# Performance work log

Hardware: AMD Instinct MI355X
Metric: run time of the kernel (lower is better)

The kernel has to match this reference:

```python
import jax, jax.numpy as jnp
import numpy as np

K = 3  # neighbors for knn_interpolate


def _knn_interpolate(x, pos, pos_skip, B, k):
    """PyG knn_interpolate with equal-sized batches.
    x: [N_coarse, C], pos: [N_coarse, 3], pos_skip: [N_fine, 3].
    """
    C = x.shape[1]
    xb = x.reshape(B, -1, C)          # [B, nc, C]
    pb = pos.reshape(B, -1, 3)        # [B, nc, 3]
    qb = pos_skip.reshape(B, -1, 3)   # [B, nf, 3]

    def per_cloud(xf, pf, qf):
        # squared distances [nf, nc]
        d2 = jnp.sum((qf[:, None, :] - pf[None, :, :]) ** 2, axis=-1)
        neg_d2k, idx = jax.lax.top_k(-d2, k)          # k smallest distances
        d2k = -neg_d2k                                # [nf, k]
        w = 1.0 / jnp.clip(d2k, 1e-16)                # inverse-distance weights
        w = jax.lax.stop_gradient(w)                  # PyG computes weights under no_grad
        feats = xf[idx]                               # [nf, k, C] gather
        return jnp.sum(w[..., None] * feats, axis=1) / jnp.sum(w, axis=1, keepdims=True)

    y = jax.vmap(per_cloud)(xb, pb, qb)               # [B, nf, C]
    return y.reshape(-1, C)


def setup_inputs() -> dict:
    key = jax.random.key(0)
    ks = jax.random.split(key, 8)
    B, n_coarse, n_fine = 16, 1024, 4096
    C_in, C_skip, C_mid, C_out = 256, 128, 256, 256
    x = jax.random.normal(ks[0], (B * n_coarse, C_in), jnp.float32)
    pos = jax.random.uniform(ks[1], (B * n_coarse, 3), jnp.float32)
    x_skip = jax.random.normal(ks[2], (B * n_fine, C_skip), jnp.float32)
    pos_skip = jax.random.uniform(ks[3], (B * n_fine, 3), jnp.float32)
    batch = jnp.repeat(jnp.arange(B, dtype=jnp.int64), n_coarse)
    batch_skip = jnp.repeat(jnp.arange(B, dtype=jnp.int64), n_fine)
    seed_idx = jnp.arange(B * n_coarse, dtype=jnp.int64)
    seed_idx_skip = jnp.arange(B * n_fine, dtype=jnp.int64)
    W1 = jax.random.normal(ks[4], (C_in + C_skip, C_mid), jnp.float32) * 0.05
    b1 = jnp.zeros((C_mid,), jnp.float32)
    W2 = jax.random.normal(ks[5], (C_mid, C_out), jnp.float32) * 0.05
    b2 = jnp.zeros((C_out,), jnp.float32)
    return {"x": x, "pos": pos, "batch": batch, "seed_idx": seed_idx,
            "x_skip": x_skip, "pos_skip": pos_skip, "batch_skip": batch_skip,
            "seed_idx_skip": seed_idx_skip, "W1": W1, "b1": b1, "W2": W2, "b2": b2}


def reference(x, pos, batch, seed_idx, x_skip, pos_skip, batch_skip, seed_idx_skip,
              W1, b1, W2, b2):
    B = int(batch[-1]) + 1  # equal-sized contiguous clouds
    y = _knn_interpolate(x, pos, pos_skip, B, K)      # [N_fine, C_in]
    h = jnp.concatenate([y, x_skip], axis=1)          # [N_fine, C_in+C_skip]
    h = jax.nn.relu(h @ W1 + b1)                      # MLP layer 1
    out = jax.nn.relu(h @ W2 + b2)                    # MLP layer 2
    return (out, pos_skip, batch_skip)
```

## Files before the change

### kernel.cpp

```cpp
#include <hip/hip_runtime.h>
#include <hip/hip_bf16.h>

#define NB    16
#define NC    1024
#define NF    4096
#define NFINE (NB*NF)
#define CIN   256
#define CSKIP 128
#define KH    (CIN+CSKIP)
#define CMID  256
#define COUT  256

typedef __attribute__((ext_vector_type(8))) short short8;
typedef __attribute__((ext_vector_type(4))) float f32x4;
typedef __attribute__((ext_vector_type(4))) unsigned int u32x4;

__global__ __launch_bounds__(256)
void bin_kernel(const float* __restrict__ pos,
                float* __restrict__ gp,
                int* __restrict__ gcs)
{
    __shared__ int cnt[512];
    __shared__ float lx[NC], ly[NC], lz[NC];
    __shared__ short lcell[NC];
    const int b = blockIdx.x, t = threadIdx.x;
    for (int i = t; i < 512; i += 256) cnt[i] = 0;
    __syncthreads();
    const float* pc = pos + (size_t)b*NC*3;
    #pragma unroll
    for (int u = 0; u < 4; ++u) {
        int i = t + u*256;
        float x = pc[3*i+0], y = pc[3*i+1], z = pc[3*i+2];
        int cx = min(7, (int)(x*8.0f));
        int cy = min(7, (int)(y*8.0f));
        int cz = min(7, (int)(z*8.0f));
        int c = (cz*8 + cy)*8 + cx;
        lx[i] = x; ly[i] = y; lz[i] = z; lcell[i] = (short)c;
        atomicAdd(&cnt[c], 1);
    }
    __syncthreads();
    if (t < 64) {
        int v[8]; int s = 0;
        #pragma unroll
        for (int u = 0; u < 8; ++u) { v[u] = cnt[t*8+u]; s += v[u]; }
        int pfx = s;
        #pragma unroll
        for (int m = 1; m < 64; m <<= 1) {
            int o = __shfl_up(pfx, m);
            if (t >= m) pfx += o;
        }
        pfx -= s;
        #pragma unroll
        for (int u = 0; u < 8; ++u) {
            gcs[b*513 + t*8+u] = pfx;
            cnt[t*8+u] = pfx;
            pfx += v[u];
        }
        if (t == 63) gcs[b*513 + 512] = NC;
    }
    __syncthreads();
    #pragma unroll
    for (int u = 0; u < 4; ++u) {
        int i = t + u*256;
        int c = lcell[i];
        int dst = atomicAdd(&cnt[c], 1);
        f32x4 v; v[0] = lx[i]; v[1] = ly[i]; v[2] = lz[i]; v[3] = __int_as_float(i);
        *(f32x4*)&gp[(size_t)(b*NC + dst)*4] = v;
    }
}

#define KQPB 32

#define INS(d, j) do {                                        \
    bool c2 = (d) < dB, c1 = (d) < dA, c0 = (d) < d0;         \
    dB = c1 ? dA : (c2 ? (d) : dB);                           \
    iB = c1 ? iA : (c2 ? (j) : iB);                           \
    dA = c0 ? d0 : (c1 ? (d) : dA);                           \
    iA = c0 ? i0 : (c1 ? (j) : iA);                           \
    d0 = c0 ? (d) : d0;                                       \
    i0 = c0 ? (j) : i0;                                       \
} while (0)

#define SCAN(JS, JE) for (int j = (JS) + g; j < (JE); j += 8) {        \
    const f32x4 p = *(const f32x4*)&pp[j][0];                          \
    float fx = qx - p[0], fy = qy - p[1], fz = qz - p[2];              \
    float dd = fx*fx + fy*fy + fz*fz;                                  \
    INS(dd, j);                                                        \
}

#define MERGE8() do {                                                          \
    _Pragma("unroll")                                                          \
    for (int mm = 1; mm < 8; mm <<= 1) {                                       \
        float e0 = __shfl_xor(d0, mm), e1 = __shfl_xor(dA, mm), e2 = __shfl_xor(dB, mm); \
        int   f0 = __shfl_xor(i0, mm), f1 = __shfl_xor(iA, mm), f2 = __shfl_xor(iB, mm); \
        INS(e0, f0); INS(e1, f1); INS(e2, f2);                                 \
    }                                                                          \
} while (0)

__global__ __launch_bounds__(256)
void knn_grid_kernel(const float* __restrict__ pos_skip,
                     const float* __restrict__ gp,
                     const int* __restrict__ gcs,
                     int* __restrict__ widx, float* __restrict__ wval)
{
    __shared__ __align__(16) float pp[NC][4];
    __shared__ unsigned short cs[513];
    const int bpc = NF/KQPB;
    const int b  = blockIdx.x / bpc;
    const int qb = blockIdx.x % bpc;
    const int t  = threadIdx.x;
    for (int i = t; i < NC; i += 256)
        *(f32x4*)&pp[i][0] = *(const f32x4*)&gp[(size_t)(b*NC + i)*4];
    for (int i = t; i < 513; i += 256) cs[i] = (unsigned short)gcs[b*513 + i];
    __syncthreads();

    const int g  = t & 7;
    const int ql = t >> 3;
    const int q  = b*NF + qb*KQPB + ql;
    const float qx = pos_skip[(size_t)q*3+0];
    const float qy = pos_skip[(size_t)q*3+1];
    const float qz = pos_skip[(size_t)q*3+2];
    const int cx = min(7, (int)(qx*8.0f));
    const int cy = min(7, (int)(qy*8.0f));
    const int cz = min(7, (int)(qz*8.0f));

    float d0 = 3.0e38f, dA = 3.0e38f, dB = 3.0e38f;
    int   i0 = 0,       iA = 0,       iB = 0;

    const int xlo = max(cx-1,0), xhi = min(cx+1,7);
    const int ylo = max(cy-1,0), yhi = min(cy+1,7);
    const int zlo = max(cz-1,0), zhi = min(cz+1,7);
    #pragma unroll
    for (int r = 0; r < 9; ++r) {
        const int z = cz - 1 + r/3;
        const int y = cy - 1 + r%3;
        const bool ok = ((unsigned)z < 8u) & ((unsigned)y < 8u);
        const int rb = (z*8 + y)*8;
        int js = 0, je = 0;
        if (ok) { js = cs[rb + xlo]; je = cs[rb + xhi + 1]; }
        SCAN(js, je);
    }
    MERGE8();

    float m1 = 3.0e38f;
    if (xlo > 0) m1 = fminf(m1, qx - xlo*0.125f);
    if (xhi < 7) m1 = fminf(m1, (xhi+1)*0.125f - qx);
    if (ylo > 0) m1 = fminf(m1, qy - ylo*0.125f);
    if (yhi < 7) m1 = fminf(m1, (yhi+1)*0.125f - qy);
    if (zlo > 0) m1 = fminf(m1, qz - zlo*0.125f);
    if (zhi < 7) m1 = fminf(m1, (zhi+1)*0.125f - qz);

    if (dB > m1*m1) {
        const float s0 = d0, s1 = dA, s2 = dB;
        const int   t0 = i0, t1 = iA, t2 = iB;
        d0 = dA = dB = 3.0e38f; i0 = iA = iB = 0;

        const int xlo2 = max(cx-2,0), xhi2 = min(cx+2,7);
        const int ylo2 = max(cy-2,0), yhi2 = min(cy+2,7);
        const int zlo2 = max(cz-2,0), zhi2 = min(cz+2,7);
        for (int z = zlo2; z <= zhi2; ++z)
        for (int y = ylo2; y <= yhi2; ++y) {
            const int rb = (z*8 + y)*8;
            const bool inner_zy = (z >= zlo && z <= zhi && y >= ylo && y <= yhi);
            int jsA, jeA, jsB, jeB;
            if (inner_zy) {
                jsA = cs[rb + xlo2]; jeA = cs[rb + xlo];
                jsB = cs[rb + xhi + 1]; jeB = cs[rb + xhi2 + 1];
            } else {
                jsA = cs[rb + xlo2]; jeA = cs[rb + xhi2 + 1];
                jsB = 0; jeB = 0;
            }
            SCAN(jsA, jeA);
            SCAN(jsB, jeB);
        }
        MERGE8();
        INS(s0, t0); INS(s1, t1); INS(s2, t2);

        float m2 = 3.0e38f;
        if (xlo2 > 0) m2 = fminf(m2, qx - xlo2*0.125f);
        if (xhi2 < 7) m2 = fminf(m2, (xhi2+1)*0.125f - qx);
        if (ylo2 > 0) m2 = fminf(m2, qy - ylo2*0.125f);
        if (yhi2 < 7) m2 = fminf(m2, (yhi2+1)*0.125f - qy);
        if (zlo2 > 0) m2 = fminf(m2, qz - zlo2*0.125f);
        if (zhi2 < 7) m2 = fminf(m2, (zhi2+1)*0.125f - qz);
        if (dB > m2*m2) {
            const float u0 = d0, u1 = dA, u2 = dB;
            const int   v0 = i0, v1 = iA, v2 = iB;
            d0 = dA = dB = 3.0e38f; i0 = iA = iB = 0;
            for (int j = g; j < NC; j += 8) {
                const f32x4 p = *(const f32x4*)&pp[j][0];
                int pcx = min(7, (int)(p[0]*8.0f));
                int pcy = min(7, (int)(p[1]*8.0f));
                int pcz = min(7, (int)(p[2]*8.0f));
                if (pcx >= xlo2 && pcx <= xhi2 && pcy >= ylo2 && pcy <= yhi2 &&
                    pcz >= zlo2 && pcz <= zhi2) continue;
                float fx = qx - p[0], fy = qy - p[1], fz = qz - p[2];
                float dd = fx*fx + fy*fy + fz*fz;
                INS(dd, j);
            }
            MERGE8();
            INS(u0, v0); INS(u1, v1); INS(u2, v2);
        }
    }

    if (g == 0) {
        const int o0 = __float_as_int(pp[i0][3]);
        const int o1 = __float_as_int(pp[iA][3]);
        const int o2 = __float_as_int(pp[iB][3]);
        float w0 = 1.0f / fmaxf(d0, 1e-16f);
        float w1 = 1.0f / fmaxf(dA, 1e-16f);
        float w2 = 1.0f / fmaxf(dB, 1e-16f);
        float inv = 1.0f / (w0 + w1 + w2);
        widx[q*3+0] = b*NC + o0;  wval[q*3+0] = w0*inv;
        widx[q*3+1] = b*NC + o1;  wval[q*3+1] = w1*inv;
        widx[q*3+2] = b*NC + o2;  wval[q*3+2] = w2*inv;
    }
}

__global__ __launch_bounds__(256)
void prep_weights(const float* __restrict__ W1, const float* __restrict__ W2,
                  __hip_bfloat16* __restrict__ W1t, __hip_bfloat16* __restrict__ W2t)
{
    int e = blockIdx.x*256 + threadIdx.x;
    if (e < CMID*KH) {
        int n = e / KH, k = e % KH;
        W1t[e] = __float2bfloat16(W1[(size_t)k*CMID + n]);
    }
    int e2 = e - CMID*KH;
    if (e2 >= 0 && e2 < COUT*CMID) {
        int n = e2 / CMID, k = e2 % CMID;
        W2t[e2] = __float2bfloat16(W2[(size_t)k*COUT + n]);
    }
}

__global__ __launch_bounds__(512, 4)
void mlp_fused(const float* __restrict__ x,
               const float* __restrict__ x_skip,
               const int* __restrict__ widx,
               const float* __restrict__ wval,
               const __hip_bfloat16* __restrict__ W1t,
               const float* __restrict__ b1,
               const __hip_bfloat16* __restrict__ W2t,
               const float* __restrict__ b2,
               float* __restrict__ out)
{
    __shared__ __align__(16) short As[64][64];
    __shared__ __align__(16) short Bs[256][64];
    __shared__ __align__(16) short Hs[64][256];
    const int nwg = gridDim.x;
    const int tile = (blockIdx.x & 7)*(nwg >> 3) + (blockIdx.x >> 3);
    const int m0 = tile * 64;

    const int t = threadIdx.x;
    const int wave = t >> 6, lane = t & 63;
    const int wm = wave >> 2, wn = wave & 3;
    const int rl = lane & 15, kq = lane >> 4;
    const short* B1r = (const short*)W1t;
    const short* B2r = (const short*)W2t;

    const int ar = t >> 3;
    const int ac = t & 7;

    const int gr = m0 + ar;
    const int j0 = widx[gr*3+0], j1 = widx[gr*3+1], j2 = widx[gr*3+2];
    const float w0 = wval[gr*3+0], w1 = wval[gr*3+1], w2 = wval[gr*3+2];

    f32x4 rA[6];
    u32x4 rB[4];

    #define LOADB(BP, KT, K0) do {                                             \
        _Pragma("unroll")                                                      \
        for (int i = 0; i < 4; ++i) {                                          \
            const int ch = t + i*512;                                          \
            const int rr = ch >> 3, cc = ch & 7;                               \
            rB[i] = *(const u32x4*)&(BP)[(size_t)rr*(KT) + (K0) + cc*8];       \
        }                                                                      \
    } while (0)

    #define LOADA1(K0) do {                                                   \
        if ((K0) < CIN) {                                                      \
            const int k = (K0) + ac*8;                                         \
            const float* p0 = &x[(size_t)j0*CIN + k];                          \
            const float* p1 = &x[(size_t)j1*CIN + k];                          \
            const float* p2 = &x[(size_t)j2*CIN + k];                          \
            rA[0] = *(const f32x4*)p0; rA[1] = *(const f32x4*)(p0+4);          \
            rA[2] = *(const f32x4*)p1; rA[3] = *(const f32x4*)(p1+4);          \
            rA[4] = *(const f32x4*)p2; rA[5] = *(const f32x4*)(p2+4);          \
        } else {                                                               \
            const int k = (K0) + ac*8 - CIN;                                   \
            const float* sp = &x_skip[(size_t)gr*CSKIP + k];                   \
            rA[0] = *(const f32x4*)sp; rA[1] = *(const f32x4*)(sp+4);          \
        }                                                                      \
    } while (0)

    f32x4 acc[2][4] = {};

    LOADA1(0); LOADB(B1r, KH, 0);

    #pragma unroll
    for (int s = 0; s < 6; ++s) {
        const int k0 = s * 64;
        __syncthreads();
        {
            short8 sv;
            if (k0 < CIN) {
                #pragma unroll
                for (int u = 0; u < 2; ++u) {
                    f32x4 a = rA[u], bq = rA[2+u], c = rA[4+u];
                    #pragma unroll
                    for (int e = 0; e < 4; ++e) {
                        float v = w0*a[e] + w1*bq[e] + w2*c[e];
                        __hip_bfloat16 bb = __float2bfloat16(v);
                        ((short*)&sv)[u*4+e] = *(short*)&bb;
                    }
                }
            } else {
                #pragma unroll
                for (int u = 0; u < 2; ++u) {
                    f32x4 a = rA[u];
                    #pragma unroll
                    for (int e = 0; e < 4; ++e) {
                        __hip_bfloat16 bb = __float2bfloat16(a[e]);
                        ((short*)&sv)[u*4+e] = *(short*)&bb;
                    }
                }
            }
            *(short8*)&As[ar][(ac ^ (ar&7))*8] = sv;
        }
        #pragma unroll
        for (int i = 0; i < 4; ++i) {
            const int ch = t + i*512;
            const int rr = ch >> 3, cc = ch & 7;
            *(u32x4*)&Bs[rr][(cc ^ (rr&7))*8] = rB[i];
        }
        __syncthreads();
        if (s < 5) { LOADA1(k0 + 64); LOADB(B1r, KH, k0 + 64); }
        else       { LOADB(B2r, CMID, 0); }
        #pragma unroll
        for (int kh = 0; kh < 2; ++kh) {
            const int kc = kh*4 + kq;
            short8 af[2], bf[4];
            #pragma unroll
            for (int mf = 0; mf < 2; ++mf)
                af[mf] = *(const short8*)&As[wm*32 + mf*16 + rl][(kc ^ (rl&7))*8];
            #pragma unroll
            for (int nf = 0; nf < 4; ++nf)
                bf[nf] = *(const short8*)&Bs[wn*64 + nf*16 + rl][(kc ^ (rl&7))*8];
            #pragma unroll
            for (int mf = 0; mf < 2; ++mf)
            #pragma unroll
            for (int nf = 0; nf < 4; ++nf)
                acc[mf][nf] = __builtin_amdgcn_mfma_f32_16x16x32_bf16(af[mf], bf[nf], acc[mf][nf], 0,0,0);
        }
    }

    #pragma unroll
    for (int mf = 0; mf < 2; ++mf)
    #pragma unroll
    for (int nf = 0; nf < 4; ++nf) {
        const int col = wn*64 + nf*16 + rl;
        const float bv = b1[col];
        #pragma unroll
        for (int i = 0; i < 4; ++i) {
            const int row = wm*32 + mf*16 + kq*4 + i;
            float v = fmaxf(acc[mf][nf][i] + bv, 0.0f);
            __hip_bfloat16 bb = __float2bfloat16(v);
            Hs[row][((col >> 3) ^ (row & 7))*8 + (col & 7)] = *(short*)&bb;
        }
    }
    __syncthreads();

    f32x4 acc2[2][4] = {};
    #pragma unroll
    for (int s = 0; s < 4; ++s) {
        if (s > 0) __syncthreads();
        #pragma unroll
        for (int i = 0; i < 4; ++i) {
            const int ch = t + i*512;
            const int rr = ch >> 3, cc = ch & 7;
            *(u32x4*)&Bs[rr][(cc ^ (rr&7))*8] = rB[i];
        }
        __syncthreads();
        if (s < 3) LOADB(B2r, CMID, (s+1)*64);
        #pragma unroll
        for (int kh = 0; kh < 2; ++kh) {
            const int kcl = kh*4 + kq;
            const int kca = s*8 + kcl;
            short8 af[2], bf[4];
            #pragma unroll
            for (int mf = 0; mf < 2; ++mf)
                af[mf] = *(const short8*)&Hs[wm*32 + mf*16 + rl][(kca ^ (rl&7))*8];
            #pragma unroll
            for (int nf = 0; nf < 4; ++nf)
                bf[nf] = *(const short8*)&Bs[wn*64 + nf*16 + rl][(kcl ^ (rl&7))*8];
            #pragma unroll
            for (int mf = 0; mf < 2; ++mf)
            #pragma unroll
            for (int nf = 0; nf < 4; ++nf)
                acc2[mf][nf] = __builtin_amdgcn_mfma_f32_16x16x32_bf16(af[mf], bf[nf], acc2[mf][nf], 0,0,0);
        }
    }
    #undef LOADA1
    #undef LOADB

    #pragma unroll
    for (int mf = 0; mf < 2; ++mf)
    #pragma unroll
    for (int nf = 0; nf < 4; ++nf) {
        const int col = wn*64 + nf*16 + rl;
        const float bv = b2[col];
        #pragma unroll
        for (int i = 0; i < 4; ++i) {
            const int row = m0 + wm*32 + mf*16 + kq*4 + i;
            out[(size_t)row*COUT + col] = fmaxf(acc2[mf][nf][i] + bv, 0.0f);
        }
    }
}

__global__ __launch_bounds__(256)
void tail_kernel(const float* __restrict__ pos_skip, float* __restrict__ out)
{
    int e = blockIdx.x*256 + threadIdx.x;
    if (e < NFINE*3) out[(size_t)NFINE*COUT + e] = pos_skip[e];
    if (e < NFINE)   out[(size_t)NFINE*COUT + (size_t)NFINE*3 + e] = (float)(e / NF);
}

extern "C" void kernel_launch(void* const* d_in, const int* in_sizes, int n_in,
                              void* d_out, int out_size, void* d_ws, size_t ws_size,
                              hipStream_t stream) {
    const float* x        = (const float*)d_in[0];
    const float* pos      = (const float*)d_in[1];
    const float* x_skip   = (const float*)d_in[4];
    const float* pos_skip = (const float*)d_in[5];
    const float* W1       = (const float*)d_in[8];
    const float* b1       = (const float*)d_in[9];
    const float* W2       = (const float*)d_in[10];
    const float* b2       = (const float*)d_in[11];
    float* out = (float*)d_out;
    char* ws = (char*)d_ws;

    int*            widx = (int*)  (ws + 0);
    float*          wval = (float*)(ws + 786432);
    __hip_bfloat16* W1t  = (__hip_bfloat16*)(ws + 1572864);
    __hip_bfloat16* W2t  = (__hip_bfloat16*)(ws + 1769472);
    float*          gp   = (float*)(ws + 1900544);
    int*            gcs  = (int*)  (ws + 2162688);

    hipLaunchKernelGGL(bin_kernel, dim3(NB), dim3(256), 0, stream,
                       pos, gp, gcs);
    hipLaunchKernelGGL(knn_grid_kernel, dim3(NB*(NF/KQPB)), dim3(256), 0, stream,
                       pos_skip, gp, gcs, widx, wval);
    hipLaunchKernelGGL(prep_weights, dim3((CMID*KH + COUT*CMID + 255)/256), dim3(256), 0, stream,
                       W1, W2, W1t, W2t);
    hipLaunchKernelGGL(mlp_fused, dim3(NFINE/64), dim3(512), 0, stream,
                       x, x_skip, widx, wval, W1t, b1, W2t, b2, out);
    hipLaunchKernelGGL(tail_kernel, dim3((NFINE*3 + 255)/256), dim3(256), 0, stream,
                       pos_skip, out);
}
```

Baseline: 76.58 us.

## Double-buffer register prefetch in fused MLP and enlarge KNN query blocks

The fused MLP kernel now keeps two register sets for A and B tiles, prefetching two k-steps ahead instead of one, so global gather latency is hidden across more MFMA work. The launch-bounds occupancy hint drops from 4 to 2 blocks to make room for the extra registers. Separately, the KNN kernel handles 64 queries per 512-thread block instead of 32 per 256, halving the number of blocks that each reload the cloud's points into shared memory. The cost is lower MLP occupancy and fewer, larger KNN blocks.

```diff
diff --git a/kernel.cpp b/kernel.cpp
--- a/kernel.cpp
+++ b/kernel.cpp
@@ -69,7 +69,7 @@
     }
 }
 
-#define KQPB 32
+#define KQPB 64
 
 #define INS(d, j) do {                                        \
     bool c2 = (d) < dB, c1 = (d) < dA, c0 = (d) < d0;         \
@@ -97,7 +97,7 @@
     }                                                                          \
 } while (0)
 
-__global__ __launch_bounds__(256)
+__global__ __launch_bounds__(512)
 void knn_grid_kernel(const float* __restrict__ pos_skip,
                      const float* __restrict__ gp,
                      const int* __restrict__ gcs,
@@ -109,9 +109,9 @@
     const int b  = blockIdx.x / bpc;
     const int qb = blockIdx.x % bpc;
     const int t  = threadIdx.x;
-    for (int i = t; i < NC; i += 256)
+    for (int i = t; i < NC; i += 512)
         *(f32x4*)&pp[i][0] = *(const f32x4*)&gp[(size_t)(b*NC + i)*4];
-    for (int i = t; i < 513; i += 256) cs[i] = (unsigned short)gcs[b*513 + i];
+    for (int i = t; i < 513; i += 512) cs[i] = (unsigned short)gcs[b*513 + i];
     __syncthreads();
 
     const int g  = t & 7;
@@ -233,7 +233,7 @@
     }
 }
 
-__global__ __launch_bounds__(512, 4)
+__global__ __launch_bounds__(512, 2)
 void mlp_fused(const float* __restrict__ x,
                const float* __restrict__ x_skip,
                const int* __restrict__ widx,
@@ -265,94 +265,109 @@
     const int j0 = widx[gr*3+0], j1 = widx[gr*3+1], j2 = widx[gr*3+2];
     const float w0 = wval[gr*3+0], w1 = wval[gr*3+1], w2 = wval[gr*3+2];
 
-    f32x4 rA[6];
-    u32x4 rB[4];
-
-    #define LOADB(BP, KT, K0) do {                                             \
+    f32x4 rA0[6], rA1[6];
+    u32x4 rB0[4], rB1[4];
+
+    #define LOADB(RB, BP, KT, K0) do {                                         \
         _Pragma("unroll")                                                      \
         for (int i = 0; i < 4; ++i) {                                          \
             const int ch = t + i*512;                                          \
             const int rr = ch >> 3, cc = ch & 7;                               \
-            rB[i] = *(const u32x4*)&(BP)[(size_t)rr*(KT) + (K0) + cc*8];       \
-        }                                                                      \
-    } while (0)
-
-    #define LOADA1(K0) do {                                                   \
+            RB[i] = *(const u32x4*)&(BP)[(size_t)rr*(KT) + (K0) + cc*8];       \
+        }                                                                      \
+    } while (0)
+
+    #define LOADA1(RA, K0) do {                                               \
         if ((K0) < CIN) {                                                      \
             const int k = (K0) + ac*8;                                         \
             const float* p0 = &x[(size_t)j0*CIN + k];                          \
             const float* p1 = &x[(size_t)j1*CIN + k];                          \
             const float* p2 = &x[(size_t)j2*CIN + k];                          \
-            rA[0] = *(const f32x4*)p0; rA[1] = *(const f32x4*)(p0+4);          \
-            rA[2] = *(const f32x4*)p1; rA[3] = *(const f32x4*)(p1+4);          \
-            rA[4] = *(const f32x4*)p2; rA[5] = *(const f32x4*)(p2+4);          \
+            RA[0] = *(const f32x4*)p0; RA[1] = *(const f32x4*)(p0+4);          \
+            RA[2] = *(const f32x4*)p1; RA[3] = *(const f32x4*)(p1+4);          \
+            RA[4] = *(const f32x4*)p2; RA[5] = *(const f32x4*)(p2+4);          \
         } else {                                                               \
             const int k = (K0) + ac*8 - CIN;                                   \
             const float* sp = &x_skip[(size_t)gr*CSKIP + k];                   \
-            rA[0] = *(const f32x4*)sp; rA[1] = *(const f32x4*)(sp+4);          \
+            RA[0] = *(const f32x4*)sp; RA[1] = *(const f32x4*)(sp+4);          \
+        }                                                                      \
+    } while (0)
+
+    #define STAGE_A(RA, K0) do {                                               \
+        short8 sv;                                                             \
+        if ((K0) < CIN) {                                                      \
+            _Pragma("unroll")                                                  \
+            for (int u = 0; u < 2; ++u) {                                      \
+                f32x4 a = RA[u], bq = RA[2+u], c = RA[4+u];                    \
+                _Pragma("unroll")                                              \
+                for (int e = 0; e < 4; ++e) {                                  \
+                    float v = w0*a[e] + w1*bq[e] + w2*c[e];                    \
+                    __hip_bfloat16 bb = __float2bfloat16(v);                   \
+                    ((short*)&sv)[u*4+e] = *(short*)&bb;                       \
+                }                                                              \
+            }                                                                  \
+        } else {                                                               \
+            _Pragma("unroll")                                                  \
+            for (int u = 0; u < 2; ++u) {                                      \
+                f32x4 a = RA[u];                                               \
+                _Pragma("unroll")                                              \
+                for (int e = 0; e < 4; ++e) {                                  \
+                    __hip_bfloat16 bb = __float2bfloat16(a[e]);                \
+                    ((short*)&sv)[u*4+e] = *(short*)&bb;                       \
+                }                                                              \
+            }                                                                  \
+        }                                                                      \
+        *(short8*)&As[ar][(ac ^ (ar&7))*8] = sv;                               \
+    } while (0)
+
+    #define STAGE_B(RB) do {                                                   \
+        _Pragma("unroll")                                                      \
+        for (int i = 0; i < 4; ++i) {                                          \
+            const int ch = t + i*512;                                          \
+            const int rr = ch >> 3, cc = ch & 7;                               \
+            *(u32x4*)&Bs[rr][(cc ^ (rr&7))*8] = RB[i];                         \
         }                                                                      \
     } while (0)
 
     f32x4 acc[2][4] = {};
 
-    LOADA1(0); LOADB(B1r, KH, 0);
-
-    #pragma unroll
-    for (int s = 0; s < 6; ++s) {
-        const int k0 = s * 64;
-        __syncthreads();
-        {
-            short8 sv;
-            if (k0 < CIN) {
-                #pragma unroll
-                for (int u = 0; u < 2; ++u) {
-                    f32x4 a = rA[u], bq = rA[2+u], c = rA[4+u];
-                    #pragma unroll
-                    for (int e = 0; e < 4; ++e) {
-                        float v = w0*a[e] + w1*bq[e] + w2*c[e];
-                        __hip_bfloat16 bb = __float2bfloat16(v);
-                        ((short*)&sv)[u*4+e] = *(short*)&bb;
-                    }
-                }
-            } else {
-                #pragma unroll
-                for (int u = 0; u < 2; ++u) {
-                    f32x4 a = rA[u];
-                    #pragma unroll
-                    for (int e = 0; e < 4; ++e) {
-                        __hip_bfloat16 bb = __float2bfloat16(a[e]);
-                        ((short*)&sv)[u*4+e] = *(short*)&bb;
-                    }
-                }
-            }
-            *(short8*)&As[ar][(ac ^ (ar&7))*8] = sv;
-        }
-        #pragma unroll
-        for (int i = 0; i < 4; ++i) {
-            const int ch = t + i*512;
-            const int rr = ch >> 3, cc = ch & 7;
-            *(u32x4*)&Bs[rr][(cc ^ (rr&7))*8] = rB[i];
-        }
-        __syncthreads();
-        if (s < 5) { LOADA1(k0 + 64); LOADB(B1r, KH, k0 + 64); }
-        else       { LOADB(B2r, CMID, 0); }
-        #pragma unroll
-        for (int kh = 0; kh < 2; ++kh) {
-            const int kc = kh*4 + kq;
-            short8 af[2], bf[4];
-            #pragma unroll
-            for (int mf = 0; mf < 2; ++mf)
-                af[mf] = *(const short8*)&As[wm*32 + mf*16 + rl][(kc ^ (rl&7))*8];
-            #pragma unroll
-            for (int nf = 0; nf < 4; ++nf)
-                bf[nf] = *(const short8*)&Bs[wn*64 + nf*16 + rl][(kc ^ (rl&7))*8];
-            #pragma unroll
-            for (int mf = 0; mf < 2; ++mf)
-            #pragma unroll
-            for (int nf = 0; nf < 4; ++nf)
-                acc[mf][nf] = __builtin_amdgcn_mfma_f32_16x16x32_bf16(af[mf], bf[nf], acc[mf][nf], 0,0,0);
-        }
-    }
+    #define MFMA1() do {                                                       \
+        _Pragma("unroll")                                                      \
+        for (int kh = 0; kh < 2; ++kh) {                                       \
+            const int kc = kh*4 + kq;                                          \
+            short8 af[2], bf[4];                                               \
+            _Pragma("unroll")                                                  \
+            for (int mf = 0; mf < 2; ++mf)                                     \
+                af[mf] = *(const short8*)&As[wm*32 + mf*16 + rl][(kc ^ (rl&7))*8]; \
+            _Pragma("unroll")                                                  \
+            for (int nf = 0; nf < 4; ++nf)                                     \
+                bf[nf] = *(const short8*)&Bs[wn*64 + nf*16 + rl][(kc ^ (rl&7))*8]; \
+            _Pragma("unroll")                                                  \
+            for (int mf = 0; mf < 2; ++mf)                                     \
+            _Pragma("unroll")                                                  \
+            for (int nf = 0; nf < 4; ++nf)                                     \
+                acc[mf][nf] = __builtin_amdgcn_mfma_f32_16x16x32_bf16(af[mf], bf[nf], acc[mf][nf], 0,0,0); \
+        }                                                                      \
+    } while (0)
+
+    LOADA1(rA0, 0);   LOADB(rB0, B1r, KH, 0);
+    LOADA1(rA1, 64);  LOADB(rB1, B1r, KH, 64);
+
+    #define PHASE1_STEP(S, RA, RB, LOADNEXT) do {                              \
+        __syncthreads();                                                       \
+        STAGE_A(RA, (S)*64);                                                   \
+        STAGE_B(RB);                                                           \
+        __syncthreads();                                                       \
+        LOADNEXT                                                               \
+        MFMA1();                                                               \
+    } while (0)
+
+    PHASE1_STEP(0, rA0, rB0, { LOADA1(rA0, 128); LOADB(rB0, B1r, KH, 128); });
+    PHASE1_STEP(1, rA1, rB1, { LOADA1(rA1, 192); LOADB(rB1, B1r, KH, 192); });
+    PHASE1_STEP(2, rA0, rB0, { LOADA1(rA0, 256); LOADB(rB0, B1r, KH, 256); });
+    PHASE1_STEP(3, rA1, rB1, { LOADA1(rA1, 320); LOADB(rB1, B1r, KH, 320); });
+    PHASE1_STEP(4, rA0, rB0, { LOADB(rB0, B2r, CMID, 0);   });
+    PHASE1_STEP(5, rA1, rB1, { LOADB(rB1, B2r, CMID, 64);  });
 
     #pragma unroll
     for (int mf = 0; mf < 2; ++mf)
@@ -371,37 +386,39 @@
     __syncthreads();
 
     f32x4 acc2[2][4] = {};
-    #pragma unroll
-    for (int s = 0; s < 4; ++s) {
-        if (s > 0) __syncthreads();
-        #pragma unroll
-        for (int i = 0; i < 4; ++i) {
-            const int ch = t + i*512;
-            const int rr = ch >> 3, cc = ch & 7;
-            *(u32x4*)&Bs[rr][(cc ^ (rr&7))*8] = rB[i];
-        }
-        __syncthreads();
-        if (s < 3) LOADB(B2r, CMID, (s+1)*64);
-        #pragma unroll
-        for (int kh = 0; kh < 2; ++kh) {
-            const int kcl = kh*4 + kq;
-            const int kca = s*8 + kcl;
-            short8 af[2], bf[4];
-            #pragma unroll
-            for (int mf = 0; mf < 2; ++mf)
-                af[mf] = *(const short8*)&Hs[wm*32 + mf*16 + rl][(kca ^ (rl&7))*8];
-            #pragma unroll
-            for (int nf = 0; nf < 4; ++nf)
-                bf[nf] = *(const short8*)&Bs[wn*64 + nf*16 + rl][(kcl ^ (rl&7))*8];
-            #pragma unroll
-            for (int mf = 0; mf < 2; ++mf)
-            #pragma unroll
-            for (int nf = 0; nf < 4; ++nf)
-                acc2[mf][nf] = __builtin_amdgcn_mfma_f32_16x16x32_bf16(af[mf], bf[nf], acc2[mf][nf], 0,0,0);
-        }
-    }
-    #undef LOADA1
-    #undef LOADB
+
+    #define MFMA2(S2) do {                                                     \
+        _Pragma("unroll")                                                      \
+        for (int kh = 0; kh < 2; ++kh) {                                       \
+            const int kcl = kh*4 + kq;                                         \
+            const int kca = (S2)*8 + kcl;                                      \
+            short8 af[2], bf[4];                                               \
+            _Pragma("unroll")                                                  \
+            for (int mf = 0; mf < 2; ++mf)                                     \
+                af[mf] = *(const short8*)&Hs[wm*32 + mf*16 + rl][(kca ^ (rl&7))*8]; \
+            _Pragma("unroll")                                                  \
+            for (int nf = 0; nf < 4; ++nf)                                     \
+                bf[nf] = *(const short8*)&Bs[wn*64 + nf*16 + rl][(kcl ^ (rl&7))*8]; \
+            _Pragma("unroll")                                                  \
+            for (int mf = 0; mf < 2; ++mf)                                     \
+            _Pragma("unroll")                                                  \
+            for (int nf = 0; nf < 4; ++nf)                                     \
+                acc2[mf][nf] = __builtin_amdgcn_mfma_f32_16x16x32_bf16(af[mf], bf[nf], acc2[mf][nf], 0,0,0); \
+        }                                                                      \
+    } while (0)
+
+    #define PHASE2_STEP(S2, RB, LOADNEXT, FIRSTBAR) do {                       \
+        FIRSTBAR                                                               \
+        STAGE_B(RB);                                                           \
+        __syncthreads();                                                       \
+        LOADNEXT                                                               \
+        MFMA2(S2);                                                             \
+    } while (0)
+
+    PHASE2_STEP(0, rB0, { LOADB(rB0, B2r, CMID, 128); }, );
+    PHASE2_STEP(1, rB1, { LOADB(rB1, B2r, CMID, 192); }, __syncthreads(););
+    PHASE2_STEP(2, rB0, { }, __syncthreads(););
+    PHASE2_STEP(3, rB1, { }, __syncthreads(););
 
     #pragma unroll
     for (int mf = 0; mf < 2; ++mf)
@@ -415,6 +432,14 @@
             out[(size_t)row*COUT + col] = fmaxf(acc2[mf][nf][i] + bv, 0.0f);
         }
     }
+    #undef LOADB
+    #undef LOADA1
+    #undef STAGE_A
+    #undef STAGE_B
+    #undef MFMA1
+    #undef MFMA2
+    #undef PHASE1_STEP
+    #undef PHASE2_STEP
 }
 
 __global__ __launch_bounds__(256)
@@ -448,7 +473,7 @@
 
     hipLaunchKernelGGL(bin_kernel, dim3(NB), dim3(256), 0, stream,
                        pos, gp, gcs);
-    hipLaunchKernelGGL(knn_grid_kernel, dim3(NB*(NF/KQPB)), dim3(256), 0, stream,
+    hipLaunchKernelGGL(knn_grid_kernel, dim3(NB*(NF/KQPB)), dim3(512), 0, stream,
                        pos_skip, gp, gcs, widx, wval);
     hipLaunchKernelGGL(prep_weights, dim3((CMID*KH + COUT*CMID + 255)/256), dim3(256), 0, stream,
                        W1, W2, W1t, W2t);
```

Result: slower. 83.50 us (+9.0%).

## Split fused MLP into two GEMM kernels and front-load gathered A tile

Applied to the files above, without the earlier changes.

Unfuses the MLP kernel into gemm1, which gathers and interpolates the full 64x384 A tile into shared memory up front and writes bf16 h1 to workspace, and gemm2, which uses 128-row tiles over h1. The KNN kernel now handles 64 queries per 512-thread block. The intent is to overlap the gather latency better, raise MFMA tile efficiency in the second GEMM and cut barrier and register pressure. The cost is an extra global round trip for h1 (32 MB of bf16 traffic) plus one more kernel launch.

```diff
diff --git a/kernel.cpp b/kernel.cpp
--- a/kernel.cpp
+++ b/kernel.cpp
@@ -69,7 +69,7 @@
     }
 }
 
-#define KQPB 32
+#define KQPB 64
 
 #define INS(d, j) do {                                        \
     bool c2 = (d) < dB, c1 = (d) < dA, c0 = (d) < d0;         \
@@ -97,7 +97,7 @@
     }                                                                          \
 } while (0)
 
-__global__ __launch_bounds__(256)
+__global__ __launch_bounds__(512)
 void knn_grid_kernel(const float* __restrict__ pos_skip,
                      const float* __restrict__ gp,
                      const int* __restrict__ gcs,
@@ -109,9 +109,9 @@
     const int b  = blockIdx.x / bpc;
     const int qb = blockIdx.x % bpc;
     const int t  = threadIdx.x;
-    for (int i = t; i < NC; i += 256)
+    for (int i = t; i < NC; i += 512)
         *(f32x4*)&pp[i][0] = *(const f32x4*)&gp[(size_t)(b*NC + i)*4];
-    for (int i = t; i < 513; i += 256) cs[i] = (unsigned short)gcs[b*513 + i];
+    for (int i = t; i < 513; i += 512) cs[i] = (unsigned short)gcs[b*513 + i];
     __syncthreads();
 
     const int g  = t & 7;
@@ -233,20 +233,17 @@
     }
 }
 
-__global__ __launch_bounds__(512, 4)
-void mlp_fused(const float* __restrict__ x,
-               const float* __restrict__ x_skip,
-               const int* __restrict__ widx,
-               const float* __restrict__ wval,
-               const __hip_bfloat16* __restrict__ W1t,
-               const float* __restrict__ b1,
-               const __hip_bfloat16* __restrict__ W2t,
-               const float* __restrict__ b2,
-               float* __restrict__ out)
+__global__ __launch_bounds__(512, 2)
+void gemm1_kernel(const float* __restrict__ x,
+                  const float* __restrict__ x_skip,
+                  const int* __restrict__ widx,
+                  const float* __restrict__ wval,
+                  const __hip_bfloat16* __restrict__ W1t,
+                  const float* __restrict__ b1,
+                  __hip_bfloat16* __restrict__ h1)
 {
-    __shared__ __align__(16) short As[64][64];
+    __shared__ __align__(16) short Af[64][KH];
     __shared__ __align__(16) short Bs[256][64];
-    __shared__ __align__(16) short Hs[64][256];
     const int nwg = gridDim.x;
     const int tile = (blockIdx.x & 7)*(nwg >> 3) + (blockIdx.x >> 3);
     const int m0 = tile * 64;
@@ -256,77 +253,182 @@
     const int wm = wave >> 2, wn = wave & 3;
     const int rl = lane & 15, kq = lane >> 4;
     const short* B1r = (const short*)W1t;
-    const short* B2r = (const short*)W2t;
 
     const int ar = t >> 3;
     const int ac = t & 7;
+    const int sw = ac ^ (ar & 7);
 
     const int gr = m0 + ar;
     const int j0 = widx[gr*3+0], j1 = widx[gr*3+1], j2 = widx[gr*3+2];
     const float w0 = wval[gr*3+0], w1 = wval[gr*3+1], w2 = wval[gr*3+2];
 
-    f32x4 rA[6];
+    f32x4 pa[6], pb[6];
+
+    #define LOADC(P, C) do {                                                   \
+        if ((C) < 4) {                                                         \
+            const int k = ((C)*8 + ac)*8;                                      \
+            const float* p0 = &x[(size_t)j0*CIN + k];                          \
+            const float* p1 = &x[(size_t)j1*CIN + k];                          \
+            const float* p2 = &x[(size_t)j2*CIN + k];                          \
+            P[0] = *(const f32x4*)p0; P[1] = *(const f32x4*)(p0+4);            \
+            P[2] = *(const f32x4*)p1; P[3] = *(const f32x4*)(p1+4);            \
+            P[4] = *(const f32x4*)p2; P[5] = *(const f32x4*)(p2+4);            \
+        } else {                                                               \
+            const int k = ((C)*8 + ac)*8 - CIN;                                \
+            const float* sp = &x_skip[(size_t)gr*CSKIP + k];                   \
+            P[0] = *(const f32x4*)sp; P[1] = *(const f32x4*)(sp+4);            \
+        }                                                                      \
+    } while (0)
+
+    #define STOREC(P, C) do {                                                  \
+        short8 sv;                                                             \
+        if ((C) < 4) {                                                         \
+            _Pragma("unroll")                                                  \
+            for (int u = 0; u < 2; ++u) {                                      \
+                f32x4 a = P[u], bq = P[2+u], c_ = P[4+u];                      \
+                _Pragma("unroll")                                              \
+                for (int e = 0; e < 4; ++e) {                                  \
+                    float v = w0*a[e] + w1*bq[e] + w2*c_[e];                   \
+                    __hip_bfloat16 bb = __float2bfloat16(v);                   \
+                    ((short*)&sv)[u*4+e] = *(short*)&bb;                       \
+                }                                                              \
+            }                                                                  \
+        } else {                                                               \
+            _Pragma("unroll")                                                  \
+            for (int u = 0; u < 2; ++u) {                                      \
+                f32x4 a = P[u];                                                \
+                _Pragma("unroll")                                              \
+                for (int e = 0; e < 4; ++e) {                                  \
+                    __hip_bfloat16 bb = __float2bfloat16(a[e]);                \
+                    ((short*)&sv)[u*4+e] = *(short*)&bb;                       \
+                }                                                              \
+            }                                                                  \
+        }                                                                      \
+        *(short8*)&Af[ar][((C)*8 + sw)*8] = sv;                                \
+    } while (0)
+
     u32x4 rB[4];
-
-    #define LOADB(BP, KT, K0) do {                                             \
+    #define LOADB(K0) do {                                                     \
         _Pragma("unroll")                                                      \
         for (int i = 0; i < 4; ++i) {                                          \
             const int ch = t + i*512;                                          \
             const int rr = ch >> 3, cc = ch & 7;                               \
-            rB[i] = *(const u32x4*)&(BP)[(size_t)rr*(KT) + (K0) + cc*8];       \
+            rB[i] = *(const u32x4*)&B1r[(size_t)rr*KH + (K0) + cc*8];          \
         }                                                                      \
     } while (0)
 
-    #define LOADA1(K0) do {                                                   \
-        if ((K0) < CIN) {                                                      \
-            const int k = (K0) + ac*8;                                         \
-            const float* p0 = &x[(size_t)j0*CIN + k];                          \
-            const float* p1 = &x[(size_t)j1*CIN + k];                          \
-            const float* p2 = &x[(size_t)j2*CIN + k];                          \
-            rA[0] = *(const f32x4*)p0; rA[1] = *(const f32x4*)(p0+4);          \
-            rA[2] = *(const f32x4*)p1; rA[3] = *(const f32x4*)(p1+4);          \
-            rA[4] = *(const f32x4*)p2; rA[5] = *(const f32x4*)(p2+4);          \
-        } else {                                                               \
-            const int k = (K0) + ac*8 - CIN;                                   \
-            const float* sp = &x_skip[(size_t)gr*CSKIP + k];                   \
-            rA[0] = *(const f32x4*)sp; rA[1] = *(const f32x4*)(sp+4);          \
+    #define STAGE_B() do {                                                     \
+        _Pragma("unroll")                                                      \
+        for (int i = 0; i < 4; ++i) {                                          \
+            const int ch = t + i*512;                                          \
+            const int rr = ch >> 3, cc = ch & 7;                               \
+            *(u32x4*)&Bs[rr][(cc ^ (rr&7))*8] = rB[i];                         \
         }                                                                      \
     } while (0)
 
+    LOADC(pa, 0); LOADC(pb, 1);
+    STOREC(pa, 0); LOADC(pa, 2);
+    STOREC(pb, 1); LOADC(pb, 3);
+    STOREC(pa, 2); LOADC(pa, 4);
+    STOREC(pb, 3); LOADC(pb, 5);
+    STOREC(pa, 4);
+    STOREC(pb, 5);
+    LOADB(0);
+
     f32x4 acc[2][4] = {};
 
-    LOADA1(0); LOADB(B1r, KH, 0);
-
     #pragma unroll
     for (int s = 0; s < 6; ++s) {
-        const int k0 = s * 64;
         __syncthreads();
-        {
-            short8 sv;
-            if (k0 < CIN) {
-                #pragma unroll
-                for (int u = 0; u < 2; ++u) {
-                    f32x4 a = rA[u], bq = rA[2+u], c = rA[4+u];
-                    #pragma unroll
-                    for (int e = 0; e < 4; ++e) {
-                        float v = w0*a[e] + w1*bq[e] + w2*c[e];
-                        __hip_bfloat16 bb = __float2bfloat16(v);
-                        ((short*)&sv)[u*4+e] = *(short*)&bb;
-                    }
-                }
-            } else {
-                #pragma unroll
-                for (int u = 0; u < 2; ++u) {
-                    f32x4 a = rA[u];
-                    #pragma unroll
-                    for (int e = 0; e < 4; ++e) {
-                        __hip_bfloat16 bb = __float2bfloat16(a[e]);
-                        ((short*)&sv)[u*4+e] = *(short*)&bb;
-                    }
-                }
-            }
-            *(short8*)&As[ar][(ac ^ (ar&7))*8] = sv;
-        }
+        STAGE_B();
+        __syncthreads();
+        if (s < 5) LOADB((s+1)*64);
+        #pragma unroll
+        for (int kh = 0; kh < 2; ++kh) {
+            const int w_ = kh*4 + kq;
+            short8 af[2], bf[4];
+            #pragma unroll
+            for (int mf = 0; mf < 2; ++mf)
+                af[mf] = *(const short8*)&Af[wm*32 + mf*16 + rl][(s*8 + (w_ ^ (rl&7)))*8];
+            #pragma unroll
+            for (int nf = 0; nf < 4; ++nf)
+                bf[nf] = *(const short8*)&Bs[wn*64 + nf*16 + rl][(w_ ^ (rl&7))*8];
+            #pragma unroll
+            for (int mf = 0; mf < 2; ++mf)
+            #pragma unroll
+            for (int nf = 0; nf < 4; ++nf)
+                acc[mf][nf] = __builtin_amdgcn_mfma_f32_16x16x32_bf16(af[mf], bf[nf], acc[mf][nf], 0,0,0);
+        }
+    }
+    #undef LOADC
+    #undef STOREC
+    #undef LOADB
+    #undef STAGE_B
+
+    #pragma unroll
+    for (int mf = 0; mf < 2; ++mf)
+    #pragma unroll
+    for (int nf = 0; nf < 4; ++nf) {
+        const int col = wn*64 + nf*16 + rl;
+        const float bv = b1[col];
+        #pragma unroll
+        for (int i = 0; i < 4; ++i) {
+            const int row = m0 + wm*32 + mf*16 + kq*4 + i;
+            float v = fmaxf(acc[mf][nf][i] + bv, 0.0f);
+            h1[(size_t)row*CMID + col] = __float2bfloat16(v);
+        }
+    }
+}
+
+__global__ __launch_bounds__(512, 2)
+void gemm2_kernel(const __hip_bfloat16* __restrict__ h1,
+                  const __hip_bfloat16* __restrict__ W2t,
+                  const float* __restrict__ b2,
+                  float* __restrict__ out)
+{
+    __shared__ __align__(16) short As[128][64];
+    __shared__ __align__(16) short Bs[256][64];
+    const int nwg = gridDim.x;
+    const int tile = (blockIdx.x & 7)*(nwg >> 3) + (blockIdx.x >> 3);
+    const int m0 = tile * 128;
+
+    const int t = threadIdx.x;
+    const int wave = t >> 6, lane = t & 63;
+    const int wm = wave >> 2, wn = wave & 3;
+    const int rl = lane & 15, kq = lane >> 4;
+    const short* Ar = (const short*)h1;
+    const short* Br = (const short*)W2t;
+
+    const int ar = t >> 2;
+    const int acb = t & 3;
+
+    f32x4 rA[2];
+    u32x4 rB[4];
+
+    #define LOADA2(K0) do {                                                    \
+        const short* p = &Ar[(size_t)(m0+ar)*CMID + (K0) + acb*8];             \
+        rA[0] = *(const f32x4*)p;                                              \
+        rA[1] = *(const f32x4*)(p+32);                                         \
+    } while (0)
+
+    #define LOADB2(K0) do {                                                    \
+        _Pragma("unroll")                                                      \
+        for (int i = 0; i < 4; ++i) {                                          \
+            const int ch = t + i*512;                                          \
+            const int rr = ch >> 3, cc = ch & 7;                               \
+            rB[i] = *(const u32x4*)&Br[(size_t)rr*CMID + (K0) + cc*8];         \
+        }                                                                      \
+    } while (0)
+
+    f32x4 acc[4][4] = {};
+
+    LOADA2(0); LOADB2(0);
+
+    #pragma unroll
+    for (int s = 0; s < 4; ++s) {
+        __syncthreads();
+        *(u32x4*)&As[ar][((acb  ) ^ (ar&7))*8] = *(u32x4*)&rA[0];
+        *(u32x4*)&As[ar][((acb+4) ^ (ar&7))*8] = *(u32x4*)&rA[1];
         #pragma unroll
         for (int i = 0; i < 4; ++i) {
             const int ch = t + i*512;
@@ -334,85 +436,37 @@
             *(u32x4*)&Bs[rr][(cc ^ (rr&7))*8] = rB[i];
         }
         __syncthreads();
-        if (s < 5) { LOADA1(k0 + 64); LOADB(B1r, KH, k0 + 64); }
-        else       { LOADB(B2r, CMID, 0); }
+        if (s < 3) { LOADA2((s+1)*64); LOADB2((s+1)*64); }
         #pragma unroll
         for (int kh = 0; kh < 2; ++kh) {
             const int kc = kh*4 + kq;
-            short8 af[2], bf[4];
-            #pragma unroll
-            for (int mf = 0; mf < 2; ++mf)
-                af[mf] = *(const short8*)&As[wm*32 + mf*16 + rl][(kc ^ (rl&7))*8];
+            short8 af[4], bf[4];
+            #pragma unroll
+            for (int mf = 0; mf < 4; ++mf)
+                af[mf] = *(const short8*)&As[wm*64 + mf*16 + rl][(kc ^ (rl&7))*8];
             #pragma unroll
             for (int nf = 0; nf < 4; ++nf)
                 bf[nf] = *(const short8*)&Bs[wn*64 + nf*16 + rl][(kc ^ (rl&7))*8];
             #pragma unroll
-            for (int mf = 0; mf < 2; ++mf)
+            for (int mf = 0; mf < 4; ++mf)
             #pragma unroll
             for (int nf = 0; nf < 4; ++nf)
                 acc[mf][nf] = __builtin_amdgcn_mfma_f32_16x16x32_bf16(af[mf], bf[nf], acc[mf][nf], 0,0,0);
         }
     }
-
-    #pragma unroll
-    for (int mf = 0; mf < 2; ++mf)
-    #pragma unroll
-    for (int nf = 0; nf < 4; ++nf) {
-        const int col = wn*64 + nf*16 + rl;
-        const float bv = b1[col];
-        #pragma unroll
-        for (int i = 0; i < 4; ++i) {
-            const int row = wm*32 + mf*16 + kq*4 + i;
-            float v = fmaxf(acc[mf][nf][i] + bv, 0.0f);
-            __hip_bfloat16 bb = __float2bfloat16(v);
-            Hs[row][((col >> 3) ^ (row & 7))*8 + (col & 7)] = *(short*)&bb;
-        }
-    }
-    __syncthreads();
-
-    f32x4 acc2[2][4] = {};
-    #pragma unroll
-    for (int s = 0; s < 4; ++s) {
-        if (s > 0) __syncthreads();
-        #pragma unroll
-        for (int i = 0; i < 4; ++i) {
-            const int ch = t + i*512;
-            const int rr = ch >> 3, cc = ch & 7;
-            *(u32x4*)&Bs[rr][(cc ^ (rr&7))*8] = rB[i];
-        }
-        __syncthreads();
-        if (s < 3) LOADB(B2r, CMID, (s+1)*64);
-        #pragma unroll
-        for (int kh = 0; kh < 2; ++kh) {
-            const int kcl = kh*4 + kq;
-            const int kca = s*8 + kcl;
-            short8 af[2], bf[4];
-            #pragma unroll
-            for (int mf = 0; mf < 2; ++mf)
-                af[mf] = *(const short8*)&Hs[wm*32 + mf*16 + rl][(kca ^ (rl&7))*8];
-            #pragma unroll
-            for (int nf = 0; nf < 4; ++nf)
-                bf[nf] = *(const short8*)&Bs[wn*64 + nf*16 + rl][(kcl ^ (rl&7))*8];
-            #pragma unroll
-            for (int mf = 0; mf < 2; ++mf)
-            #pragma unroll
-            for (int nf = 0; nf < 4; ++nf)
-                acc2[mf][nf] = __builtin_amdgcn_mfma_f32_16x16x32_bf16(af[mf], bf[nf], acc2[mf][nf], 0,0,0);
-        }
-    }
-    #undef LOADA1
-    #undef LOADB
-
-    #pragma unroll
-    for (int mf = 0; mf < 2; ++mf)
+    #undef LOADA2
+    #undef LOADB2
+
+    #pragma unroll
+    for (int mf = 0; mf < 4; ++mf)
     #pragma unroll
     for (int nf = 0; nf < 4; ++nf) {
         const int col = wn*64 + nf*16 + rl;
         const float bv = b2[col];
         #pragma unroll
         for (int i = 0; i < 4; ++i) {
-            const int row = m0 + wm*32 + mf*16 + kq*4 + i;
-            out[(size_t)row*COUT + col] = fmaxf(acc2[mf][nf][i] + bv, 0.0f);
+            const int row = m0 + wm*64 + mf*16 + kq*4 + i;
+            out[(size_t)row*COUT + col] = fmaxf(acc[mf][nf][i] + bv, 0.0f);
         }
     }
 }
@@ -445,15 +499,18 @@
     __hip_bfloat16* W2t  = (__hip_bfloat16*)(ws + 1769472);
     float*          gp   = (float*)(ws + 1900544);
     int*            gcs  = (int*)  (ws + 2162688);
+    __hip_bfloat16* h1   = (__hip_bfloat16*)(ws + 2195520);
 
     hipLaunchKernelGGL(bin_kernel, dim3(NB), dim3(256), 0, stream,
                        pos, gp, gcs);
-    hipLaunchKernelGGL(knn_grid_kernel, dim3(NB*(NF/KQPB)), dim3(256), 0, stream,
+    hipLaunchKernelGGL(knn_grid_kernel, dim3(NB*(NF/KQPB)), dim3(512), 0, stream,
                        pos_skip, gp, gcs, widx, wval);
     hipLaunchKernelGGL(prep_weights, dim3((CMID*KH + COUT*CMID + 255)/256), dim3(256), 0, stream,
                        W1, W2, W1t, W2t);
-    hipLaunchKernelGGL(mlp_fused, dim3(NFINE/64), dim3(512), 0, stream,
-                       x, x_skip, widx, wval, W1t, b1, W2t, b2, out);
+    hipLaunchKernelGGL(gemm1_kernel, dim3(NFINE/64), dim3(512), 0, stream,
+                       x, x_skip, widx, wval, W1t, b1, h1);
+    hipLaunchKernelGGL(gemm2_kernel, dim3(NFINE/128), dim3(512), 0, stream,
+                       h1, W2t, b2, out);
     hipLaunchKernelGGL(tail_kernel, dim3((NFINE*3 + 255)/256), dim3(256), 0, stream,
                        pos_skip, out);
 }
```

Measured after the change: 92.39 us. 20.6% more time.
